# Performance work log

Hardware: AMD Instinct MI355X
Metric: run time of the kernel (lower is better)

Reference implementation:

```python
import jax, jax.numpy as jnp
import numpy as np


def setup_inputs() -> dict:
    key = jax.random.key(0)
    k1, k2, k3, k4, k5 = jax.random.split(key, 5)
    N, C, H, W, HID = 32, 3, 64, 64, 256
    x = jax.random.normal(k1, (N, C, H, W), dtype=jnp.float32)
    w_xh = jax.random.normal(k2, (HID, C), dtype=jnp.float32) * (1.0 / np.sqrt(C))
    b_xh = jax.random.normal(k3, (HID,), dtype=jnp.float32) * 0.02
    w_hh = jax.random.normal(k4, (HID, HID), dtype=jnp.float32) * (1.0 / np.sqrt(HID))
    b_hh = jax.random.normal(k5, (HID,), dtype=jnp.float32) * 0.02
    return {"x": x, "w_xh": w_xh, "b_xh": b_xh, "w_hh": w_hh, "b_hh": b_hh}


def reference(x, w_xh, b_xh, w_hh, b_hh):
    N, C, H, W = x.shape
    HID = w_hh.shape[0]
    # 1x1 convs as einsums
    xh = jnp.einsum('nchw,oc->nohw', x, w_xh) + b_xh[None, :, None, None]
    # h=None -> zeros; fc_hh(zeros) = bias broadcast
    h0 = jnp.broadcast_to(b_hh[None, :, None, None], xh.shape).astype(xh.dtype)
    # shifted neighbor views (zero-padded)
    hl = jnp.pad(h0, ((0, 0), (0, 0), (0, 0), (1, 0)))[..., :-1]   # left neighbor
    hr = jnp.pad(h0, ((0, 0), (0, 0), (0, 0), (0, 1)))[..., 1:]    # right neighbor
    ht = jnp.pad(h0, ((0, 0), (0, 0), (1, 0), (0, 0)))[:, :, :-1]  # top neighbor
    cols_even = (jnp.arange(W) % 2 == 0)
    h = jnp.where(cols_even[None, None, None, :], hl, hr) + ht
    nl = jnp.pad(xh, ((0, 0), (0, 0), (0, 0), (1, 0)))[..., :-1]
    nr = jnp.pad(xh, ((0, 0), (0, 0), (0, 0), (0, 1)))[..., 1:]
    nt = jnp.pad(xh, ((0, 0), (0, 0), (1, 0), (0, 0)))[:, :, :-1]
    nb = jnp.pad(xh, ((0, 0), (0, 0), (0, 1), (0, 0)))[:, :, 1:]
    n = nl + nr + nt + nb
    logit = jnp.transpose(h + n, (2, 3, 0, 1))  # [H, W, N, HID]

    col_idx = jnp.arange(W)

    def col_step(h_prev, xs):
        l_j, j = xs                                 # l_j: [N, HID]
        contrib = h_prev @ w_hh.T + b_hh            # F.linear
        l = l_j + jnp.where(j == 0, 0.0, 1.0) * contrib
        h_new = jax.nn.sigmoid(l)
        return h_new, h_new

    def row_step(h_below, xs):
        l_row, k = xs                               # l_row: [W, N, HID], k=0 is bottom row
        i = H - 1 - k
        below = jnp.einsum('wnh,gh->wng', h_below, w_hh) + b_hh
        l_row = l_row + jnp.where(k == 0, 0.0, 1.0) * below
        flip = (i % 2 == 0)                         # even rows scanned right-to-left
        l_dir = jnp.where(flip, l_row[::-1], l_row)
        _, h_dir = jax.lax.scan(col_step, jnp.zeros((N, HID), l_row.dtype), (l_dir, col_idx))
        h_row = jnp.where(flip, h_dir[::-1], h_dir)
        return h_row, h_row

    logit_btm_up = logit[::-1]                      # rows processed bottom-up
    _, rows = jax.lax.scan(row_step, jnp.zeros((W, N, HID), logit.dtype),
                           (logit_btm_up, jnp.arange(H)))
    h_next = rows[::-1]                             # [H, W, N, HID] in row order
    return jnp.transpose(h_next, (2, 3, 0, 1))      # [N, HID, H, W]
```

## Files before the change

kernel.cpp:

```cpp
#include <hip/hip_runtime.h>

#define HID 256
#define HH  64
#define WW  64

typedef _Float16 f16x8 __attribute__((ext_vector_type(8)));
typedef float    f32x4 __attribute__((ext_vector_type(4)));

#define LDS_BARRIER() do {                                   \
    asm volatile("s_waitcnt lgkmcnt(0)" ::: "memory");       \
    __builtin_amdgcn_sched_barrier(0);                       \
    __builtin_amdgcn_s_barrier();                            \
    __builtin_amdgcn_sched_barrier(0);                       \
  } while (0)

__global__ __launch_bounds__(1024, 4)
void mrf_scan_kernel(const float* __restrict__ x,
                     const float* __restrict__ w_xh,
                     const float* __restrict__ b_xh,
                     const float* __restrict__ w_hh,
                     const float* __restrict__ b_hh,
                     float* __restrict__ out)
{
    const int n   = blockIdx.x;
    const int tid = threadIdx.x;
    const int wv  = tid >> 6;
    const int l   = tid & 63;
    const int l15 = l & 15;
    const int lq  = l >> 4;
    const int oc  = wv * 16 + l15;

    __shared__ __align__(16) _Float16 hbel[WW][HID];
    __shared__ __align__(16) _Float16 hsum[2][HID];
    __shared__ __align__(16) float4   xs4[WW];

    {
        unsigned int* z = (unsigned int*)(&hbel[0][0]);
        #pragma unroll
        for (int q = 0; q < (WW*HID/2)/1024; ++q) z[tid + 1024*q] = 0u;
        if (tid < 256) ((unsigned int*)(&hsum[0][0]))[tid] = 0u;
    }

    f16x8 Bf[8];
    {
        const float* wr = w_hh + (size_t)oc * HID;
        #pragma unroll
        for (int kf = 0; kf < 8; ++kf) {
            const int g0 = kf*32 + lq*8;
            f16x8 b;
            #pragma unroll
            for (int j = 0; j < 8; ++j) b[j] = (_Float16)wr[g0 + j];
            Bf[kf] = b;
        }
    }

    const float wx0 = w_xh[oc*3+0];
    const float wx1 = w_xh[oc*3+1];
    const float wx2 = w_xh[oc*3+2];
    const float bx  = b_xh[oc];
    const float bh  = b_hh[oc];

    const int    XP = HH*WW;
    const float* xn = x + (size_t)n * 3 * XP;
    float* outc = out + (size_t)n * HID * XP + (size_t)oc * XP;

    __syncthreads();

    int cur = 0;
    bool     pend = false;
    float    s_pend = 0.f;
    _Float16 h16_pend = (_Float16)0.f;
    float*   optr_pend = outc;
    _Float16* hbptr_pend = &hbel[0][0];

    for (int k = 0; k < HH; ++k) {
        const int i    = HH - 1 - k;
        const int flip = ((i & 1) == 0);

        if (tid < 192) {
            const int c = tid >> 6, w = tid & 63;
            const float* xc = xn + (size_t)c * XP;
            float s = 0.f;
            if (w > 0)    s += xc[i*WW + w - 1];
            if (w < WW-1) s += xc[i*WW + w + 1];
            if (i > 0)    s += xc[(i-1)*WW + w];
            if (i < HH-1) s += xc[(i+1)*WW + w];
            ((float*)&xs4[w])[c] = s;
            if (c == 0) {
                const float cnt = (float)((w>0) + (w<WW-1) + (i>0) + (i<HH-1));
                ((float*)&xs4[w])[3] = cnt;
            }
        }
        LDS_BARRIER();

        const float Fr = ((i != 0) ? 1.f : 0.f) + ((k != 0) ? 1.f : 0.f);
        float* orow = outc + (size_t)i * WW;

        for (int t = 0; t < WW; ++t) {
            const int w  = flip ? (WW-1-t) : t;
            const int wn = (t < WW-1) ? (flip ? (WW-2-t) : (t+1)) : w;

            if (pend && lq == 0) {
                *hbptr_pend = h16_pend;
                *optr_pend  = s_pend;
            }

            f16x8 Af[8];
            #pragma unroll
            for (int kf = 0; kf < 8; ++kf)
                Af[kf] = *(const f16x8*)((const char*)(&hsum[cur][0]) + kf*64 + lq*16);

            _Float16 hb = (_Float16)0.f;
            if (lq == 0) hb = hbel[wn][oc];

            f32x4 cA = (f32x4){0.f,0.f,0.f,0.f};
            f32x4 cB = (f32x4){0.f,0.f,0.f,0.f};
            #pragma unroll
            for (int kf = 0; kf < 4; ++kf) {
                cA = __builtin_amdgcn_mfma_f32_16x16x32_f16(Af[kf],   Bf[kf],   cA, 0, 0, 0);
                cB = __builtin_amdgcn_mfma_f32_16x16x32_f16(Af[kf+4], Bf[kf+4], cB, 0, 0, 0);
            }

            float s = 0.f; _Float16 h16 = (_Float16)0.f;
            if (lq == 0) {
                const float4 xv = xs4[w];
                const float Ft = Fr + ((t != 0 && t != WW-1) ? 1.f : 0.f)
                                    + ((t != 0) ? 1.f : 0.f);
                float pre = xv.w * bx;
                pre = fmaf(xv.x, wx0, pre);
                pre = fmaf(xv.y, wx1, pre);
                pre = fmaf(xv.z, wx2, pre);
                pre = fmaf(Ft,   bh,  pre);

                const float val = cA[0] + cB[0] + pre;
                const float e   = __expf(-val);
                s   = __builtin_amdgcn_rcpf(1.f + e);
                h16 = (_Float16)s;
                hsum[cur ^ 1][oc] = (t < WW-1) ? (_Float16)(h16 + hb) : h16;
            }

            LDS_BARRIER();

            pend = true;
            s_pend = s; h16_pend = h16;
            hbptr_pend = &hbel[w][oc];
            optr_pend  = orow + w;
            cur ^= 1;
        }
    }

    if (lq == 0) *optr_pend = s_pend;
}

extern "C" void kernel_launch(void* const* d_in, const int* in_sizes, int n_in,
                              void* d_out, int out_size, void* d_ws, size_t ws_size,
                              hipStream_t stream) {
    const float* x    = (const float*)d_in[0];
    const float* w_xh = (const float*)d_in[1];
    const float* b_xh = (const float*)d_in[2];
    const float* w_hh = (const float*)d_in[3];
    const float* b_hh = (const float*)d_in[4];
    float* out = (float*)d_out;
    (void)in_sizes; (void)n_in; (void)d_ws; (void)ws_size; (void)out_size;

    mrf_scan_kernel<<<dim3(32), dim3(1024), 0, stream>>>(x, w_xh, b_xh, w_hh, b_hh, out);
}
```

Measured before the change: 2.289 ms.

## Halve block to 8 waves, each computing 32 output channels per step

The block shrinks from 16 to 8 wavefronts, and each wave now computes two 16-channel tiles of the recurrent matvec using 8 MFMAs per tile. Each MFMA pair starts from a fresh zero accumulator, so the dependent accumulation chains are shorter, and the pointwise sigmoid math runs on all lanes rather than only a quarter of them. The deferred hbel/output stores are replaced by direct stores before the per-column barrier. The intent is to cut the barrier cost across fewer waves and shorten the per-column serial latency, at the price of twice the MFMA work per wave and more registers for weights.

```diff
diff --git a/kernel.cpp b/kernel.cpp
--- a/kernel.cpp
+++ b/kernel.cpp
@@ -14,7 +14,7 @@
     __builtin_amdgcn_sched_barrier(0);                       \
   } while (0)
 
-__global__ __launch_bounds__(1024, 4)
+__global__ __launch_bounds__(512, 2)
 void mrf_scan_kernel(const float* __restrict__ x,
                      const float* __restrict__ w_xh,
                      const float* __restrict__ b_xh,
@@ -28,7 +28,9 @@
     const int l   = tid & 63;
     const int l15 = l & 15;
     const int lq  = l >> 4;
-    const int oc  = wv * 16 + l15;
+    const int cb  = wv * 32;
+    const int oc  = cb + (lq >> 1) * 16 + l15;
+    const bool writer = ((lq & 1) == 0);
 
     __shared__ __align__(16) _Float16 hbel[WW][HID];
     __shared__ __align__(16) _Float16 hsum[2][HID];
@@ -37,20 +39,21 @@
     {
         unsigned int* z = (unsigned int*)(&hbel[0][0]);
         #pragma unroll
-        for (int q = 0; q < (WW*HID/2)/1024; ++q) z[tid + 1024*q] = 0u;
+        for (int q = 0; q < (WW*HID/2)/512; ++q) z[tid + 512*q] = 0u;
         if (tid < 256) ((unsigned int*)(&hsum[0][0]))[tid] = 0u;
     }
 
-    f16x8 Bf[8];
-    {
-        const float* wr = w_hh + (size_t)oc * HID;
+    f16x8 Bf[2][8];
+    #pragma unroll
+    for (int tt = 0; tt < 2; ++tt) {
+        const float* wr = w_hh + (size_t)(cb + tt*16 + l15) * HID;
         #pragma unroll
         for (int kf = 0; kf < 8; ++kf) {
             const int g0 = kf*32 + lq*8;
             f16x8 b;
             #pragma unroll
             for (int j = 0; j < 8; ++j) b[j] = (_Float16)wr[g0 + j];
-            Bf[kf] = b;
+            Bf[tt][kf] = b;
         }
     }
 
@@ -62,17 +65,11 @@
 
     const int    XP = HH*WW;
     const float* xn = x + (size_t)n * 3 * XP;
-    float* outc = out + (size_t)n * HID * XP + (size_t)oc * XP;
+    float*     outc = out + (size_t)n * HID * XP + (size_t)oc * XP;
 
     __syncthreads();
 
     int cur = 0;
-    bool     pend = false;
-    float    s_pend = 0.f;
-    _Float16 h16_pend = (_Float16)0.f;
-    float*   optr_pend = outc;
-    _Float16* hbptr_pend = &hbel[0][0];
-
     for (int k = 0; k < HH; ++k) {
         const int i    = HH - 1 - k;
         const int flip = ((i & 1) == 0);
@@ -100,56 +97,51 @@
             const int w  = flip ? (WW-1-t) : t;
             const int wn = (t < WW-1) ? (flip ? (WW-2-t) : (t+1)) : w;
 
-            if (pend && lq == 0) {
-                *hbptr_pend = h16_pend;
-                *optr_pend  = s_pend;
-            }
-
+            const float4 xv = xs4[w];
             f16x8 Af[8];
             #pragma unroll
             for (int kf = 0; kf < 8; ++kf)
                 Af[kf] = *(const f16x8*)((const char*)(&hsum[cur][0]) + kf*64 + lq*16);
+            const _Float16 hb = hbel[wn][oc];
 
-            _Float16 hb = (_Float16)0.f;
-            if (lq == 0) hb = hbel[wn][oc];
+            const float Ft = Fr + ((t != 0 && t != WW-1) ? 1.f : 0.f) + ((t != 0) ? 1.f : 0.f);
+            float pre = xv.w * bx;
+            pre = fmaf(xv.x, wx0, pre);
+            pre = fmaf(xv.y, wx1, pre);
+            pre = fmaf(xv.z, wx2, pre);
+            pre = fmaf(Ft,   bh,  pre);
 
-            f32x4 cA = (f32x4){0.f,0.f,0.f,0.f};
-            f32x4 cB = (f32x4){0.f,0.f,0.f,0.f};
+            f32x4 cs[2][4];
             #pragma unroll
-            for (int kf = 0; kf < 4; ++kf) {
-                cA = __builtin_amdgcn_mfma_f32_16x16x32_f16(Af[kf],   Bf[kf],   cA, 0, 0, 0);
-                cB = __builtin_amdgcn_mfma_f32_16x16x32_f16(Af[kf+4], Bf[kf+4], cB, 0, 0, 0);
-            }
+            for (int tt = 0; tt < 2; ++tt)
+                #pragma unroll
+                for (int j = 0; j < 4; ++j) {
+                    f32x4 z0 = (f32x4){0.f,0.f,0.f,0.f};
+                    z0 = __builtin_amdgcn_mfma_f32_16x16x32_f16(Af[2*j],   Bf[tt][2*j],   z0, 0, 0, 0);
+                    cs[tt][j] = __builtin_amdgcn_mfma_f32_16x16x32_f16(Af[2*j+1], Bf[tt][2*j+1], z0, 0, 0, 0);
+                }
 
-            float s = 0.f; _Float16 h16 = (_Float16)0.f;
-            if (lq == 0) {
-                const float4 xv = xs4[w];
-                const float Ft = Fr + ((t != 0 && t != WW-1) ? 1.f : 0.f)
-                                    + ((t != 0) ? 1.f : 0.f);
-                float pre = xv.w * bx;
-                pre = fmaf(xv.x, wx0, pre);
-                pre = fmaf(xv.y, wx1, pre);
-                pre = fmaf(xv.z, wx2, pre);
-                pre = fmaf(Ft,   bh,  pre);
+            float tot[2];
+            #pragma unroll
+            for (int tt = 0; tt < 2; ++tt)
+                tot[tt] = (cs[tt][0][0] + cs[tt][1][0]) + (cs[tt][2][0] + cs[tt][3][0]);
+            const float dot = ((lq >> 1) == 0) ? tot[0] : tot[1];
 
-                const float val = cA[0] + cB[0] + pre;
-                const float e   = __expf(-val);
-                s   = __builtin_amdgcn_rcpf(1.f + e);
-                h16 = (_Float16)s;
+            const float val = dot + pre;
+            const float e   = __expf(-val);
+            const float s   = __builtin_amdgcn_rcpf(1.f + e);
+
+            const _Float16 h16 = (_Float16)s;
+            if (writer) {
+                hbel[w][oc] = h16;
                 hsum[cur ^ 1][oc] = (t < WW-1) ? (_Float16)(h16 + hb) : h16;
+                orow[w] = s;
             }
 
             LDS_BARRIER();
-
-            pend = true;
-            s_pend = s; h16_pend = h16;
-            hbptr_pend = &hbel[w][oc];
-            optr_pend  = orow + w;
             cur ^= 1;
         }
     }
-
-    if (lq == 0) *optr_pend = s_pend;
 }
 
 extern "C" void kernel_launch(void* const* d_in, const int* in_sizes, int n_in,
@@ -163,5 +155,5 @@
     float* out = (float*)d_out;
     (void)in_sizes; (void)n_in; (void)d_ws; (void)ws_size; (void)out_size;
 
-    mrf_scan_kernel<<<dim3(32), dim3(1024), 0, stream>>>(x, w_xh, b_xh, w_hh, b_hh, out);
+    mrf_scan_kernel<<<dim3(32), dim3(512), 0, stream>>>(x, w_xh, b_xh, w_hh, b_hh, out);
 }
```

Measured after the change: 1.933 ms. -15.6%, faster.
